# Kernel optimization log

Measured on AMD Instinct MI355X. Metric: run time of the kernel, lower is better.

The kernel has to match this reference:

```python
import jax, jax.numpy as jnp
import numpy as np

ALPHA = 0.25
GAMMA = 2.0
B, A, C, M = 8, 120000, 80, 32


def setup_inputs() -> dict:
    key = jax.random.key(0)
    k1, k2, k3, k4, k5, k6 = jax.random.split(key, 6)
    classifications = jax.random.uniform(k1, (B, A, C), jnp.float32)
    regressions = jax.random.normal(k2, (B, A, 4), jnp.float32)
    # anchors: valid x1<x2, y1<y2 boxes in a 1024x1024 image
    cx = jax.random.uniform(k3, (A,), jnp.float32, 0.0, 1024.0)
    cy = jax.random.uniform(k4, (A,), jnp.float32, 0.0, 1024.0)
    w = jax.random.uniform(jax.random.fold_in(k3, 1), (A,), jnp.float32, 16.0, 256.0)
    h = jax.random.uniform(jax.random.fold_in(k4, 1), (A,), jnp.float32, 16.0, 256.0)
    anchors = jnp.stack([cx - 0.5 * w, cy - 0.5 * h, cx + 0.5 * w, cy + 0.5 * h], axis=1)[None]
    # annotations: [x1,y1,x2,y2,label], all valid (label in [0, C))
    gcx = jax.random.uniform(k5, (B, M), jnp.float32, 64.0, 960.0)
    gcy = jax.random.uniform(jax.random.fold_in(k5, 1), (B, M), jnp.float32, 64.0, 960.0)
    gw = jax.random.uniform(jax.random.fold_in(k5, 2), (B, M), jnp.float32, 16.0, 256.0)
    gh = jax.random.uniform(jax.random.fold_in(k5, 3), (B, M), jnp.float32, 16.0, 256.0)
    labels = jax.random.randint(k6, (B, M), 0, C).astype(jnp.float32)
    annotations = jnp.stack(
        [gcx - 0.5 * gw, gcy - 0.5 * gh, gcx + 0.5 * gw, gcy + 0.5 * gh, labels], axis=2)
    return dict(classifications=classifications, regressions=regressions,
                anchors=anchors, annotations=annotations)


def _calc_iou(a, b):
    # a: [A,4] anchors, b: [M,4] gt boxes -> [A,M]
    area = (b[:, 2] - b[:, 0]) * (b[:, 3] - b[:, 1])
    iw = jnp.minimum(a[:, 2, None], b[None, :, 2]) - jnp.maximum(a[:, 0, None], b[None, :, 0])
    ih = jnp.minimum(a[:, 3, None], b[None, :, 3]) - jnp.maximum(a[:, 1, None], b[None, :, 1])
    inter = jnp.clip(iw, 0.0) * jnp.clip(ih, 0.0)
    ua = ((a[:, 2] - a[:, 0]) * (a[:, 3] - a[:, 1]))[:, None] + area[None, :] - inter
    return inter / jnp.clip(ua, 1e-8)


def _per_image(cls, reg, annots, anchor):
    valid = annots[:, 4] != -1.0  # padded gt boxes (label == -1) are ignored
    num_valid = valid.sum()
    cls = jnp.clip(cls, 1e-4, 1.0 - 1e-4)
    iou = jnp.where(valid[None, :], _calc_iou(anchor, annots[:, :4]), -1.0)  # [A,M]
    iou_max = iou.max(axis=1)
    iou_argmax = iou.argmax(axis=1)
    positive = iou_max >= 0.5
    num_pos = positive.sum()
    assigned = annots[iou_argmax]  # [A,5]
    nclass = cls.shape[1]
    # targets: -1 ignore; 0 where IoU<0.4 or positive; one-hot 1 at gt class for positives
    targets = jnp.full(cls.shape, -1.0, cls.dtype)
    targets = jnp.where((iou_max < 0.4)[:, None], 0.0, targets)
    onehot = jax.nn.one_hot(assigned[:, 4].astype(jnp.int32), nclass, dtype=cls.dtype)
    targets = jnp.where(positive[:, None], onehot, targets)
    alpha_factor = jnp.where(targets == 1.0, ALPHA, 1.0 - ALPHA)
    focal_w = alpha_factor * jnp.where(targets == 1.0, 1.0 - cls, cls) ** GAMMA
    bce = -(targets * jnp.log(cls) + (1.0 - targets) * jnp.log(1.0 - cls))
    cls_loss_mat = jnp.where(targets != -1.0, focal_w * bce, 0.0)
    npos_f = num_pos.astype(cls.dtype)
    cls_loss = cls_loss_mat.sum() / jnp.maximum(npos_f, 1.0)
    aw = anchor[:, 2] - anchor[:, 0]
    ah = anchor[:, 3] - anchor[:, 1]
    acx = anchor[:, 0] + 0.5 * aw
    acy = anchor[:, 1] + 0.5 * ah
    gw = assigned[:, 2] - assigned[:, 0]
    gh = assigned[:, 3] - assigned[:, 1]
    gcx = assigned[:, 0] + 0.5 * gw
    gcy = assigned[:, 1] + 0.5 * gh
    gw = jnp.maximum(gw, 1.0)
    gh = jnp.maximum(gh, 1.0)
    t = jnp.stack([(gcx - acx) / aw, (gcy - acy) / ah,
                   jnp.log(gw / aw), jnp.log(gh / ah)], axis=1)
    t = t / jnp.array([[0.1, 0.1, 0.2, 0.2]], t.dtype)
    diff = jnp.abs(t - reg)
    rl = jnp.where(diff <= 1.0 / 9.0, 0.5 * 9.0 * diff * diff, diff - 0.5 / 9.0)
    rl = jnp.where(positive[:, None], rl, 0.0)
    reg_loss = rl.sum() / jnp.maximum(npos_f * 4.0, 1.0)  # mean over [num_pos,4]
    reg_loss = jnp.where(num_pos > 0, reg_loss, 0.0)
    has = num_valid > 0
    return jnp.where(has, cls_loss, 0.0), jnp.where(has, reg_loss, 0.0)


def reference(classifications, regressions, anchors, annotations):
    anchor = anchors[0]
    cls_l, reg_l = jax.vmap(lambda c, r, a: _per_image(c, r, a, anchor))(
        classifications, regressions, annotations)
    return cls_l.mean(keepdims=True), reg_l.mean(keepdims=True)
```

## Files before the change

### kernel.cpp

```cpp
#include <hip/hip_runtime.h>

constexpr int B_IMG = 8;
constexpr int A_N   = 120000;
constexpr int C_N   = 80;
constexpr int M_N   = 32;

constexpr float ALPHA = 0.25f;

constexpr int BLK   = 256;
constexpr int APB   = 512;
constexpr int NBLK  = (A_N + APB - 1) / APB;
constexpr int F4PA  = C_N / 4;

__device__ __forceinline__ float smooth_l1(float d) {
    d = fabsf(d);
    return (d <= (1.0f / 9.0f)) ? 4.5f * d * d : d - (0.5f / 9.0f);
}

__device__ __forceinline__ float loss_neg(float x) {
    float p = fminf(fmaxf(x, 1e-4f), 0.9999f);
    return (1.0f - ALPHA) * p * p * (-__logf(1.0f - p));
}

__device__ __forceinline__ float loss_pos(float x) {
    float p = fminf(fmaxf(x, 1e-4f), 0.9999f);
    float q = 1.0f - p;
    return ALPHA * q * q * (-__logf(p));
}

__device__ __forceinline__ signed char assign_one(
    const float4 anc, const float* __restrict__ ann,
    const float4* __restrict__ regs, int b, int a,
    float& regl, int& pcount)
{
    const float ax1 = anc.x, ay1 = anc.y, ax2 = anc.z, ay2 = anc.w;
    const float areaA = (ax2 - ax1) * (ay2 - ay1);

    float bi = -1.0f;
    float bu = 1.0f;
    int   bm = -1;
    #pragma unroll 4
    for (int m = 0; m < M_N; ++m) {
        const float gx1 = ann[m * 5 + 0];
        const float gy1 = ann[m * 5 + 1];
        const float gx2 = ann[m * 5 + 2];
        const float gy2 = ann[m * 5 + 3];
        const bool valid = (ann[m * 5 + 4] != -1.0f);
        float iw = fminf(ax2, gx2) - fmaxf(ax1, gx1);
        float ih = fminf(ay2, gy2) - fmaxf(ay1, gy1);
        iw = fmaxf(iw, 0.0f);
        ih = fmaxf(ih, 0.0f);
        const float inter = iw * ih;
        const float areaB = (gx2 - gx1) * (gy2 - gy1);
        const float ua = fmaxf(areaA + areaB - inter, 1e-8f);
        const bool better = valid && (inter * bu > bi * ua);
        if (better) { bi = inter; bu = ua; bm = m; }
    }

    const float iouMax = (bm >= 0) ? (bi / bu) : -1.0f;
    const bool positive = (iouMax >= 0.5f);

    if (positive) {
        pcount += 1;
        const float aw  = ax2 - ax1;
        const float ah  = ay2 - ay1;
        const float acx = ax1 + 0.5f * aw;
        const float acy = ay1 + 0.5f * ah;
        const float gx1 = ann[bm * 5 + 0];
        const float gy1 = ann[bm * 5 + 1];
        const float gx2 = ann[bm * 5 + 2];
        const float gy2 = ann[bm * 5 + 3];
        float gw = gx2 - gx1;
        float gh = gy2 - gy1;
        const float gcx = gx1 + 0.5f * gw;
        const float gcy = gy1 + 0.5f * gh;
        gw = fmaxf(gw, 1.0f);
        gh = fmaxf(gh, 1.0f);
        const float t0 = ((gcx - acx) / aw) * 10.0f;
        const float t1 = ((gcy - acy) / ah) * 10.0f;
        const float t2 = __logf(gw / aw) * 5.0f;
        const float t3 = __logf(gh / ah) * 5.0f;
        const float4 rg = regs[(size_t)b * A_N + a];
        regl += smooth_l1(t0 - rg.x) + smooth_l1(t1 - rg.y) +
                smooth_l1(t2 - rg.z) + smooth_l1(t3 - rg.w);
    }

    if (iouMax < 0.4f) return -1;
    if (positive)      return (signed char)(int)ann[bm * 5 + 4];
    return -2;
}

__global__ __launch_bounds__(BLK) void fused_kernel(
    const float* __restrict__ cls,
    const float* __restrict__ regressions,
    const float* __restrict__ anchors,
    const float* __restrict__ annotations,
    float* __restrict__ clsPart,
    float* __restrict__ regPart,
    float* __restrict__ nposPart)
{
    const int b    = blockIdx.y;
    const int base = blockIdx.x * APB;
    const int nA   = min(APB, A_N - base);
    const float* __restrict__ ann = annotations + (size_t)b * M_N * 5;
    const float4* __restrict__ regs = (const float4*)regressions;

    __shared__ signed char scode[APB];

    float regl = 0.0f;
    int   pcnt = 0;
    const int t = threadIdx.x;
    #pragma unroll
    for (int s = 0; s < APB; s += BLK) {
        const int li = s + t;
        const int a  = base + li;
        signed char c = -2;
        if (li < nA) {
            const float4 anc = ((const float4*)anchors)[a];
            c = assign_one(anc, ann, regs, b, a, regl, pcnt);
        }
        scode[li] = c;
    }
    __syncthreads();

    const float4* __restrict__ src =
        (const float4*)(cls + (size_t)b * A_N * C_N) + (size_t)base * F4PA;
    const int nF4 = nA * F4PA;
    float csum = 0.0f;
    for (int idx = t; idx < nF4; idx += BLK) {
        const float4 v = src[idx];
        const int al = (int)((unsigned)idx / 20u);
        const int k  = (int)((unsigned)idx % 20u) * 4;
        const int code = scode[al];
        if (code != -2) {
            float s = loss_neg(v.x) + loss_neg(v.y) + loss_neg(v.z) + loss_neg(v.w);
            const int j = code - k;
            if ((unsigned)j < 4u) {
                const float x = (j == 0) ? v.x : (j == 1) ? v.y : (j == 2) ? v.z : v.w;
                s += loss_pos(x) - loss_neg(x);
            }
            csum += s;
        }
    }

    float r = regl, p = (float)pcnt, c = csum;
    #pragma unroll
    for (int off = 32; off; off >>= 1) {
        r += __shfl_down(r, off);
        p += __shfl_down(p, off);
        c += __shfl_down(c, off);
    }
    __shared__ float wr[BLK / 64], wp[BLK / 64], wc[BLK / 64];
    const int wid = t >> 6;
    if ((t & 63) == 0) { wr[wid] = r; wp[wid] = p; wc[wid] = c; }
    __syncthreads();
    if (t == 0) {
        float rr = 0.0f, pp = 0.0f, cc = 0.0f;
        #pragma unroll
        for (int w = 0; w < BLK / 64; ++w) { rr += wr[w]; pp += wp[w]; cc += wc[w]; }
        const int pidx = b * NBLK + blockIdx.x;
        clsPart[pidx]  = cc;
        regPart[pidx]  = rr;
        nposPart[pidx] = pp;
    }
}

__global__ __launch_bounds__(64 * B_IMG) void finalize_kernel(
    const float* __restrict__ annotations,
    const float* __restrict__ clsPart,
    const float* __restrict__ regPart,
    const float* __restrict__ nposPart,
    float* __restrict__ out)
{
    const int w    = threadIdx.x >> 6;
    const int lane = threadIdx.x & 63;

    float c = 0.0f, r = 0.0f, p = 0.0f;
    for (int i = lane; i < NBLK; i += 64) {
        const int idx = w * NBLK + i;
        c += clsPart[idx];
        r += regPart[idx];
        p += nposPart[idx];
    }
    #pragma unroll
    for (int off = 32; off; off >>= 1) {
        c += __shfl_down(c, off);
        r += __shfl_down(r, off);
        p += __shfl_down(p, off);
    }

    __shared__ float sc[B_IMG], sr[B_IMG];
    if (lane == 0) {
        bool has = false;
        for (int m = 0; m < M_N; ++m)
            has = has || (annotations[(size_t)w * M_N * 5 + m * 5 + 4] != -1.0f);
        const float cl = c / fmaxf(p, 1.0f);
        const float rl = (p > 0.0f) ? r / (p * 4.0f) : 0.0f;
        sc[w] = has ? cl : 0.0f;
        sr[w] = has ? rl : 0.0f;
    }
    __syncthreads();
    if (threadIdx.x == 0) {
        float ca = 0.0f, ra = 0.0f;
        #pragma unroll
        for (int i = 0; i < B_IMG; ++i) { ca += sc[i]; ra += sr[i]; }
        out[0] = ca * (1.0f / B_IMG);
        out[1] = ra * (1.0f / B_IMG);
    }
}

extern "C" void kernel_launch(void* const* d_in, const int* in_sizes, int n_in,
                              void* d_out, int out_size, void* d_ws, size_t ws_size,
                              hipStream_t stream) {
    const float* classifications = (const float*)d_in[0];
    const float* regressions     = (const float*)d_in[1];
    const float* anchors         = (const float*)d_in[2];
    const float* annotations     = (const float*)d_in[3];
    float* out = (float*)d_out;

    float* clsPart  = (float*)d_ws;
    float* regPart  = clsPart + (size_t)B_IMG * NBLK;
    float* nposPart = regPart + (size_t)B_IMG * NBLK;

    fused_kernel<<<dim3(NBLK, B_IMG), BLK, 0, stream>>>(
        classifications, regressions, anchors, annotations,
        clsPart, regPart, nposPart);

    finalize_kernel<<<1, 64 * B_IMG, 0, stream>>>(
        annotations, clsPart, regPart, nposPart, out);
}
```

Measured before the change: 91.23 us.

## Batch classification loads with unrolled loop, mask multiply, separate positive correction

The classification pass is reworked. The positive-class correction now runs in its own per-anchor loop that gathers one element per positive anchor, so the main streaming loop is branch-free: it multiplies each float4's negative loss by a per-anchor 0/1 mask kept in shared memory. Full tiles issue eight float4 loads before computing, which raises memory-level parallelism. Launch bounds request 4 blocks per SM and the IoU/assign loop unroll factors are reduced, which lowers register pressure. In exchange the kernel now computes transcendental losses for ignored anchors that are masked to zero, and it does an extra scattered read per positive anchor.

New measurement: 78.07 us. 14.4% less time.

```diff
diff --git a/kernel.cpp b/kernel.cpp
--- a/kernel.cpp
+++ b/kernel.cpp
@@ -7,10 +7,12 @@
 
 constexpr float ALPHA = 0.25f;
 
-constexpr int BLK   = 256;
-constexpr int APB   = 512;
-constexpr int NBLK  = (A_N + APB - 1) / APB;
-constexpr int F4PA  = C_N / 4;
+constexpr int BLK    = 256;
+constexpr int APB    = 512;
+constexpr int NBLK   = (A_N + APB - 1) / APB;
+constexpr int F4PA   = C_N / 4;
+constexpr int UNROLL = 8;
+constexpr int FAST_ITERS = (APB * F4PA) / (BLK * UNROLL);
 
 __device__ __forceinline__ float smooth_l1(float d) {
     d = fabsf(d);
@@ -39,7 +41,7 @@
     float bi = -1.0f;
     float bu = 1.0f;
     int   bm = -1;
-    #pragma unroll 4
+    #pragma unroll 2
     for (int m = 0; m < M_N; ++m) {
         const float gx1 = ann[m * 5 + 0];
         const float gy1 = ann[m * 5 + 1];
@@ -90,7 +92,7 @@
     return -2;
 }
 
-__global__ __launch_bounds__(BLK) void fused_kernel(
+__global__ __launch_bounds__(BLK, 4) void fused_kernel(
     const float* __restrict__ cls,
     const float* __restrict__ regressions,
     const float* __restrict__ anchors,
@@ -106,11 +108,12 @@
     const float4* __restrict__ regs = (const float4*)regressions;
 
     __shared__ signed char scode[APB];
+    __shared__ float       smask[APB];
 
     float regl = 0.0f;
     int   pcnt = 0;
     const int t = threadIdx.x;
-    #pragma unroll
+    #pragma unroll 1
     for (int s = 0; s < APB; s += BLK) {
         const int li = s + t;
         const int a  = base + li;
@@ -120,26 +123,48 @@
             c = assign_one(anc, ann, regs, b, a, regl, pcnt);
         }
         scode[li] = c;
+        smask[li] = (c != -2) ? 1.0f : 0.0f;
     }
     __syncthreads();
 
-    const float4* __restrict__ src =
-        (const float4*)(cls + (size_t)b * A_N * C_N) + (size_t)base * F4PA;
-    const int nF4 = nA * F4PA;
+    const float* __restrict__ rowbase = cls + (size_t)(b * A_N + base) * C_N;
     float csum = 0.0f;
-    for (int idx = t; idx < nF4; idx += BLK) {
-        const float4 v = src[idx];
-        const int al = (int)((unsigned)idx / 20u);
-        const int k  = (int)((unsigned)idx % 20u) * 4;
-        const int code = scode[al];
-        if (code != -2) {
-            float s = loss_neg(v.x) + loss_neg(v.y) + loss_neg(v.z) + loss_neg(v.w);
-            const int j = code - k;
-            if ((unsigned)j < 4u) {
-                const float x = (j == 0) ? v.x : (j == 1) ? v.y : (j == 2) ? v.z : v.w;
-                s += loss_pos(x) - loss_neg(x);
+
+    #pragma unroll 1
+    for (int s = 0; s < APB; s += BLK) {
+        const int li = s + t;
+        const int code = scode[li];
+        if (code >= 0) {
+            const float x = rowbase[(size_t)li * C_N + code];
+            csum += loss_pos(x) - loss_neg(x);
+        }
+    }
+
+    const float4* __restrict__ src = (const float4*)rowbase;
+    if (nA == APB) {
+        const float4* p = src + t;
+        #pragma unroll 1
+        for (int it = 0; it < FAST_ITERS; ++it) {
+            float4 v[UNROLL];
+            #pragma unroll
+            for (int u = 0; u < UNROLL; ++u) v[u] = p[u * BLK];
+            const int ibase = it * (BLK * UNROLL) + t;
+            #pragma unroll
+            for (int u = 0; u < UNROLL; ++u) {
+                const unsigned idx = (unsigned)(ibase + u * BLK);
+                const float m = smask[idx / 20u];
+                csum += m * (loss_neg(v[u].x) + loss_neg(v[u].y) +
+                             loss_neg(v[u].z) + loss_neg(v[u].w));
             }
-            csum += s;
+            p += BLK * UNROLL;
+        }
+    } else {
+        const int nF4 = nA * F4PA;
+        for (int idx = t; idx < nF4; idx += BLK) {
+            const float4 v = src[idx];
+            const float m = smask[(unsigned)idx / 20u];
+            csum += m * (loss_neg(v.x) + loss_neg(v.y) +
+                         loss_neg(v.z) + loss_neg(v.w));
         }
     }
 
```

## Split into dense negative-loss sweep plus per-anchor correction blocks

Applied to the files above, without the earlier changes.

Restructures the fused kernel into two block roles. One set of blocks sums the negative focal term over every classification element as a flat streaming reduction with no dependence on anchor assignment. The other blocks compute IoU assignment and regression loss, then apply corrections: they subtract the row sum for ignored anchors and add the positive-minus-negative delta for positive ones. This decouples the bandwidth-bound sweep from the assignment compute so both run concurrently. The cost is re-reading the full rows of ignored anchors and a somewhat different floating-point summation order.

New measurement: 125.1 us. +37.2%, slower.

```diff
diff --git a/kernel.cpp b/kernel.cpp
--- a/kernel.cpp
+++ b/kernel.cpp
@@ -8,9 +8,15 @@
 constexpr float ALPHA = 0.25f;
 
 constexpr int BLK   = 256;
-constexpr int APB   = 512;
-constexpr int NBLK  = (A_N + APB - 1) / APB;
-constexpr int F4PA  = C_N / 4;
+constexpr int SB    = 128;
+constexpr int ApT   = 4;
+constexpr int APB   = BLK * ApT;
+constexpr int AB    = (A_N + APB - 1) / APB;
+constexpr int F4TOT = A_N * C_N / 4;
+constexpr int U     = 8;
+constexpr int CHUNK = BLK * U;
+
+typedef float f4v __attribute__((ext_vector_type(4)));
 
 __device__ __forceinline__ float smooth_l1(float d) {
     d = fabsf(d);
@@ -20,6 +26,10 @@
 __device__ __forceinline__ float loss_neg(float x) {
     float p = fminf(fmaxf(x, 1e-4f), 0.9999f);
     return (1.0f - ALPHA) * p * p * (-__logf(1.0f - p));
+}
+
+__device__ __forceinline__ float loss_neg4(f4v v) {
+    return loss_neg(v[0]) + loss_neg(v[1]) + loss_neg(v[2]) + loss_neg(v[3]);
 }
 
 __device__ __forceinline__ float loss_pos(float x) {
@@ -39,7 +49,7 @@
     float bi = -1.0f;
     float bu = 1.0f;
     int   bm = -1;
-    #pragma unroll 4
+    #pragma unroll 2
     for (int m = 0; m < M_N; ++m) {
         const float gx1 = ann[m * 5 + 0];
         const float gy1 = ann[m * 5 + 1];
@@ -90,84 +100,102 @@
     return -2;
 }
 
-__global__ __launch_bounds__(BLK) void fused_kernel(
+__global__ __launch_bounds__(BLK, 4) void fused_kernel(
     const float* __restrict__ cls,
     const float* __restrict__ regressions,
     const float* __restrict__ anchors,
     const float* __restrict__ annotations,
-    float* __restrict__ clsPart,
+    float* __restrict__ sPart,
+    float* __restrict__ corrPart,
     float* __restrict__ regPart,
     float* __restrict__ nposPart)
 {
-    const int b    = blockIdx.y;
-    const int base = blockIdx.x * APB;
-    const int nA   = min(APB, A_N - base);
-    const float* __restrict__ ann = annotations + (size_t)b * M_N * 5;
-    const float4* __restrict__ regs = (const float4*)regressions;
-
-    __shared__ signed char scode[APB];
-
-    float regl = 0.0f;
-    int   pcnt = 0;
+    const int b = blockIdx.y;
     const int t = threadIdx.x;
-    #pragma unroll
-    for (int s = 0; s < APB; s += BLK) {
-        const int li = s + t;
-        const int a  = base + li;
-        signed char c = -2;
-        if (li < nA) {
-            const float4 anc = ((const float4*)anchors)[a];
-            c = assign_one(anc, ann, regs, b, a, regl, pcnt);
-        }
-        scode[li] = c;
-    }
-    __syncthreads();
-
-    const float4* __restrict__ src =
-        (const float4*)(cls + (size_t)b * A_N * C_N) + (size_t)base * F4PA;
-    const int nF4 = nA * F4PA;
-    float csum = 0.0f;
-    for (int idx = t; idx < nF4; idx += BLK) {
-        const float4 v = src[idx];
-        const int al = (int)((unsigned)idx / 20u);
-        const int k  = (int)((unsigned)idx % 20u) * 4;
-        const int code = scode[al];
-        if (code != -2) {
-            float s = loss_neg(v.x) + loss_neg(v.y) + loss_neg(v.z) + loss_neg(v.w);
-            const int j = code - k;
-            if ((unsigned)j < 4u) {
-                const float x = (j == 0) ? v.x : (j == 1) ? v.y : (j == 2) ? v.z : v.w;
-                s += loss_pos(x) - loss_neg(x);
+    const int wave = t >> 6;
+    const int lane = t & 63;
+
+    if (blockIdx.x < SB) {
+        const int j = blockIdx.x;
+        const f4v* __restrict__ src = (const f4v*)(cls + (size_t)b * A_N * C_N);
+        float s = 0.0f;
+        #pragma unroll 1
+        for (int base = j * CHUNK; base < F4TOT; base += SB * CHUNK) {
+            if (base + CHUNK <= F4TOT) {
+                f4v v[U];
+                #pragma unroll
+                for (int u = 0; u < U; ++u) v[u] = src[base + u * BLK + t];
+                #pragma unroll
+                for (int u = 0; u < U; ++u) s += loss_neg4(v[u]);
+            } else {
+                for (int idx = base + t; idx < F4TOT; idx += BLK)
+                    s += loss_neg4(src[idx]);
             }
-            csum += s;
-        }
-    }
-
-    float r = regl, p = (float)pcnt, c = csum;
-    #pragma unroll
-    for (int off = 32; off; off >>= 1) {
-        r += __shfl_down(r, off);
-        p += __shfl_down(p, off);
-        c += __shfl_down(c, off);
-    }
-    __shared__ float wr[BLK / 64], wp[BLK / 64], wc[BLK / 64];
-    const int wid = t >> 6;
-    if ((t & 63) == 0) { wr[wid] = r; wp[wid] = p; wc[wid] = c; }
-    __syncthreads();
-    if (t == 0) {
-        float rr = 0.0f, pp = 0.0f, cc = 0.0f;
+        }
         #pragma unroll
-        for (int w = 0; w < BLK / 64; ++w) { rr += wr[w]; pp += wp[w]; cc += wc[w]; }
-        const int pidx = b * NBLK + blockIdx.x;
-        clsPart[pidx]  = cc;
-        regPart[pidx]  = rr;
-        nposPart[pidx] = pp;
+        for (int off = 32; off; off >>= 1) s += __shfl_down(s, off);
+        __shared__ float ws[BLK / 64];
+        if (lane == 0) ws[wave] = s;
+        __syncthreads();
+        if (t == 0) {
+            float ss = 0.0f;
+            #pragma unroll
+            for (int w = 0; w < BLK / 64; ++w) ss += ws[w];
+            sPart[b * SB + j] = ss;
+        }
+    } else {
+        const int j  = blockIdx.x - SB;
+        const int a0 = j * APB;
+        const float* __restrict__ ann = annotations + (size_t)b * M_N * 5;
+        const float4* __restrict__ regs = (const float4*)regressions;
+
+        float regl = 0.0f, corr = 0.0f;
+        int   pcnt = 0;
+        #pragma unroll 1
+        for (int sIt = 0; sIt < ApT; ++sIt) {
+            const int a = a0 + sIt * BLK + t;
+            if (a < A_N) {
+                const float4 anc = ((const float4*)anchors)[a];
+                const signed char code = assign_one(anc, ann, regs, b, a, regl, pcnt);
+                if (code == -2) {
+                    const f4v* __restrict__ row =
+                        (const f4v*)(cls + ((size_t)b * A_N + a) * C_N);
+                    float rs = 0.0f;
+                    #pragma unroll 4
+                    for (int u = 0; u < C_N / 4; ++u) rs += loss_neg4(row[u]);
+                    corr -= rs;
+                } else if (code >= 0) {
+                    const float x = cls[((size_t)b * A_N + a) * C_N + code];
+                    corr += loss_pos(x) - loss_neg(x);
+                }
+            }
+        }
+        float r = regl, p = (float)pcnt, c = corr;
+        #pragma unroll
+        for (int off = 32; off; off >>= 1) {
+            r += __shfl_down(r, off);
+            p += __shfl_down(p, off);
+            c += __shfl_down(c, off);
+        }
+        __shared__ float wr[BLK / 64], wp[BLK / 64], wc[BLK / 64];
+        if (lane == 0) { wr[wave] = r; wp[wave] = p; wc[wave] = c; }
+        __syncthreads();
+        if (t == 0) {
+            float rr = 0.0f, pp = 0.0f, cc = 0.0f;
+            #pragma unroll
+            for (int w = 0; w < BLK / 64; ++w) { rr += wr[w]; pp += wp[w]; cc += wc[w]; }
+            const int pidx = b * AB + j;
+            corrPart[pidx] = cc;
+            regPart[pidx]  = rr;
+            nposPart[pidx] = pp;
+        }
     }
 }
 
 __global__ __launch_bounds__(64 * B_IMG) void finalize_kernel(
     const float* __restrict__ annotations,
-    const float* __restrict__ clsPart,
+    const float* __restrict__ sPart,
+    const float* __restrict__ corrPart,
     const float* __restrict__ regPart,
     const float* __restrict__ nposPart,
     float* __restrict__ out)
@@ -175,15 +203,17 @@
     const int w    = threadIdx.x >> 6;
     const int lane = threadIdx.x & 63;
 
-    float c = 0.0f, r = 0.0f, p = 0.0f;
-    for (int i = lane; i < NBLK; i += 64) {
-        const int idx = w * NBLK + i;
-        c += clsPart[idx];
+    float s = 0.0f, c = 0.0f, r = 0.0f, p = 0.0f;
+    for (int i = lane; i < SB; i += 64) s += sPart[w * SB + i];
+    for (int i = lane; i < AB; i += 64) {
+        const int idx = w * AB + i;
+        c += corrPart[idx];
         r += regPart[idx];
         p += nposPart[idx];
     }
     #pragma unroll
     for (int off = 32; off; off >>= 1) {
+        s += __shfl_down(s, off);
         c += __shfl_down(c, off);
         r += __shfl_down(r, off);
         p += __shfl_down(p, off);
@@ -194,7 +224,7 @@
         bool has = false;
         for (int m = 0; m < M_N; ++m)
             has = has || (annotations[(size_t)w * M_N * 5 + m * 5 + 4] != -1.0f);
-        const float cl = c / fmaxf(p, 1.0f);
+        const float cl = (s + c) / fmaxf(p, 1.0f);
         const float rl = (p > 0.0f) ? r / (p * 4.0f) : 0.0f;
         sc[w] = has ? cl : 0.0f;
         sr[w] = has ? rl : 0.0f;
@@ -218,14 +248,15 @@
     const float* annotations     = (const float*)d_in[3];
     float* out = (float*)d_out;
 
-    float* clsPart  = (float*)d_ws;
-    float* regPart  = clsPart + (size_t)B_IMG * NBLK;
-    float* nposPart = regPart + (size_t)B_IMG * NBLK;
-
-    fused_kernel<<<dim3(NBLK, B_IMG), BLK, 0, stream>>>(
+    float* sPart    = (float*)d_ws;
+    float* corrPart = sPart    + (size_t)B_IMG * SB;
+    float* regPart  = corrPart + (size_t)B_IMG * AB;
+    float* nposPart = regPart  + (size_t)B_IMG * AB;
+
+    fused_kernel<<<dim3(SB + AB, B_IMG), BLK, 0, stream>>>(
         classifications, regressions, anchors, annotations,
-        clsPart, regPart, nposPart);
+        sPart, corrPart, regPart, nposPart);
 
     finalize_kernel<<<1, 64 * B_IMG, 0, stream>>>(
-        annotations, clsPart, regPart, nposPart, out);
-}
+        annotations, sPart, corrPart, regPart, nposPart, out);
+}
```
